# Performance work log

Hardware: AMD Instinct MI355X
Metric: run time of the kernel (lower is better)

The kernel has to match this reference:

```python
import jax, jax.numpy as jnp
import numpy as np

SPATIAL = ((100, 100), (50, 50), (25, 25), (13, 13))
STARTS = [0]
for _h, _w in SPATIAL[:-1]:
    STARTS.append(STARTS[-1] + _h * _w)
L_TOTAL = sum(h * w for h, w in SPATIAL)  # 13294
D, DFFN, NL, NH, NP = 256, 1024, 4, 8, 4
DH = D // NH
EPS = 1e-5


def _ln(x, g, b):
    mu = x.mean(-1, keepdims=True)
    var = ((x - mu) ** 2).mean(-1, keepdims=True)
    return (x - mu) * jax.lax.rsqrt(var + EPS) * g + b


def _bilinear(v_l, x, y, H, W):
    # v_l: [B,NH,H*W,DH]; x,y: [B,NH,Q*NP] pixel coords (grid_sample align_corners=False, zero padding)
    x0f = jnp.floor(x); y0f = jnp.floor(y)
    lx, ly = x - x0f, y - y0f
    x0 = x0f.astype(jnp.int32); y0 = y0f.astype(jnp.int32)
    acc = 0.0
    for dx, dy, w in ((0, 0, (1 - lx) * (1 - ly)), (1, 0, lx * (1 - ly)),
                      (0, 1, (1 - lx) * ly), (1, 1, lx * ly)):
        xi, yi = x0 + dx, y0 + dy
        valid = (xi >= 0) & (xi < W) & (yi >= 0) & (yi < H)
        idx = jnp.clip(yi, 0, H - 1) * W + jnp.clip(xi, 0, W - 1)
        g = jnp.take_along_axis(v_l, idx[..., None], axis=2)  # [B,NH,Q*NP,DH]
        acc = acc + g * (w * valid.astype(w.dtype))[..., None]
    return acc


def _msdeform(query, value_in, ref, norm_wh, Woff, boff, Wattn, battn, Wval, bval, Wout, bout):
    B, Q, _ = query.shape
    v = (value_in @ Wval + bval).reshape(B, L_TOTAL, NH, DH)
    off = (query @ Woff + boff).reshape(B, Q, NH, NL, NP, 2)
    aw = (query @ Wattn + battn).reshape(B, Q, NH, NL * NP)
    aw = jax.nn.softmax(aw, axis=-1).reshape(B, Q, NH, NL, NP)
    # normalized sampling locations in [0,1]: ref + offset / (W,H)
    loc = ref[:, :, None, :, None, :] + off / norm_wh[None, None, None, :, None, :]
    out = 0.0
    for l, (H, W) in enumerate(SPATIAL):
        s = STARTS[l]
        v_l = v[:, s:s + H * W].transpose(0, 2, 1, 3)          # [B,NH,HW,DH]
        loc_l = loc[:, :, :, l].transpose(0, 2, 1, 3, 4)       # [B,NH,Q,NP,2]
        x = (loc_l[..., 0] * W - 0.5).reshape(B, NH, Q * NP)
        y = (loc_l[..., 1] * H - 0.5).reshape(B, NH, Q * NP)
        samp = _bilinear(v_l, x, y, H, W).reshape(B, NH, Q, NP, DH)
        w_l = aw[:, :, :, l].transpose(0, 2, 1, 3)             # [B,NH,Q,NP]
        out = out + (samp * w_l[..., None]).sum(3)             # [B,NH,Q,DH]
    out = out.transpose(0, 2, 1, 3).reshape(B, Q, D)
    return out @ Wout + bout


def setup_inputs() -> dict:
    key = jax.random.key(0)
    ks = jax.random.split(key, 12)
    B = 4
    s = 0.02
    return {
        "src": jax.random.normal(ks[0], (B, L_TOTAL, D), jnp.float32),
        "pos": jax.random.normal(ks[1], (B, L_TOTAL, D), jnp.float32),
        "reference_points": jax.random.uniform(ks[2], (B, L_TOTAL, NL, 2), jnp.float32),
        "spatial_shapes": jnp.array(SPATIAL, jnp.int32),
        "level_start_index": jnp.array(STARTS, jnp.int32),
        "W_off": jax.random.normal(ks[3], (D, NH * NL * NP * 2), jnp.float32) * 0.01,
        "b_off": jax.random.normal(ks[4], (NH * NL * NP * 2,), jnp.float32) * 0.5,
        "W_attn": jax.random.normal(ks[5], (D, NH * NL * NP), jnp.float32) * s,
        "b_attn": jnp.zeros((NH * NL * NP,), jnp.float32),
        "W_val": jax.random.normal(ks[6], (D, D), jnp.float32) * s,
        "b_val": jnp.zeros((D,), jnp.float32),
        "W_out": jax.random.normal(ks[7], (D, D), jnp.float32) * s,
        "b_out": jnp.zeros((D,), jnp.float32),
        "ln_sa_g": jnp.ones((D,), jnp.float32),
        "ln_sa_b": jnp.zeros((D,), jnp.float32),
        "W1": jax.random.normal(ks[8], (D, DFFN), jnp.float32) * s,
        "b1": jnp.zeros((DFFN,), jnp.float32),
        "W2": jax.random.normal(ks[9], (DFFN, D), jnp.float32) * s,
        "b2": jnp.zeros((D,), jnp.float32),
        "ln_ff_g": jnp.ones((D,), jnp.float32),
        "ln_ff_b": jnp.zeros((D,), jnp.float32),
    }


def reference(src, pos, reference_points, spatial_shapes, level_start_index,
              W_off, b_off, W_attn, b_attn, W_val, b_val, W_out, b_out,
              ln_sa_g, ln_sa_b, W1, b1, W2, b2, ln_ff_g, ln_ff_b):
    # offset normalizer is (W, H) per level
    norm_wh = jnp.stack([spatial_shapes[:, 1], spatial_shapes[:, 0]], -1).astype(src.dtype)
    q = src + pos  # with_pos_embed
    sa = _msdeform(q, src, reference_points, norm_wh,
                   W_off, b_off, W_attn, b_attn, W_val, b_val, W_out, b_out)
    x = _ln(sa + src, ln_sa_g, ln_sa_b)          # dropout = identity (eval)
    y = jnp.maximum(x @ W1 + b1, 0.0) @ W2 + b2  # relu FFN
    return _ln(y + x, ln_ff_g, ln_ff_b)
```

## Files before the change

### kernel.cpp

```cpp
#include <hip/hip_runtime.h>
#include <hip/hip_bf16.h>

typedef __hip_bfloat16 bf16;
typedef short bf16x8 __attribute__((ext_vector_type(8)));
typedef float f32x4  __attribute__((ext_vector_type(4)));

#define ROWS 53176
#define LTOT 13294

__device__ __forceinline__ float b2f(bf16 v) { return __bfloat162float(v); }

__device__ __forceinline__ void gl2lds16(const void* g, void* l) {
    __builtin_amdgcn_global_load_lds(
        (const __attribute__((address_space(1))) unsigned*)g,
        (__attribute__((address_space(3))) unsigned*)l, 16, 0, 0);
}

template<bool RELU>
__global__ __launch_bounds__(256)
void mfma_gemm_n(const bf16* __restrict__ A, const bf16* __restrict__ Bt,
                 const float* __restrict__ bias, bf16* __restrict__ C,
                 int M, int N, int K)
{
    __shared__ __align__(16) short As[2][128 * 32];
    __shared__ __align__(16) short Bs[2][128 * 32];
    const int tid  = threadIdx.x;
    const int wave = tid >> 6, lane = tid & 63;

    const int nwg  = gridDim.x * gridDim.y;
    const int orig = blockIdx.y * gridDim.x + blockIdx.x;
    const int wgid = ((nwg & 7) == 0) ? ((orig & 7) * (nwg >> 3) + (orig >> 3)) : orig;
    const int bx = wgid % gridDim.x, by = wgid / gridDim.x;

    const int m0 = by * 128, n0 = bx * 128;
    const int lrow = lane >> 2, lcol = lane & 3;
    const int quad = lane >> 4, l15 = lane & 15;

    f32x4 acc[4][4];
#pragma unroll
    for (int i = 0; i < 4; ++i)
#pragma unroll
        for (int j = 0; j < 4; ++j) acc[i][j] = (f32x4){0.f, 0.f, 0.f, 0.f};

    const int wM = (wave >> 1) * 64, wN = (wave & 1) * 64;

    auto stage = [&](int p, int kk) {
#pragma unroll
        for (int q = 0; q < 2; ++q) {
            int rbase = wave * 32 + q * 16;
            int row = rbase + lrow;
            int sw = (lcol * 16) ^ ((row & 3) << 4);
            gl2lds16((const char*)(A  + (size_t)(m0 + row) * K + kk) + sw, &As[p][rbase * 32]);
            gl2lds16((const char*)(Bt + (size_t)(n0 + row) * K + kk) + sw, &Bs[p][rbase * 32]);
        }
    };

    auto compute = [&](int p) {
        bf16x8 af[4], bfr[4];
#pragma unroll
        for (int i = 0; i < 4; ++i) {
            int row = wM + i * 16 + l15;
            af[i] = *(const bf16x8*)((const char*)&As[p][row * 32]
                                     + ((quad * 16) ^ ((row & 3) << 4)));
        }
#pragma unroll
        for (int j = 0; j < 4; ++j) {
            int row = wN + j * 16 + l15;
            bfr[j] = *(const bf16x8*)((const char*)&Bs[p][row * 32]
                                      + ((quad * 16) ^ ((row & 3) << 4)));
        }
#pragma unroll
        for (int i = 0; i < 4; ++i)
#pragma unroll
            for (int j = 0; j < 4; ++j)
                acc[i][j] = __builtin_amdgcn_mfma_f32_16x16x32_bf16(bfr[j], af[i], acc[i][j], 0, 0, 0);
    };

    stage(0, 0);
    __syncthreads();
    int p = 0;
    for (int kk = 32; kk < K; kk += 32) {
        stage(p ^ 1, kk);
        compute(p);
        __syncthreads();
        p ^= 1;
    }
    compute(p);

    float4 b4[4];
#pragma unroll
    for (int j = 0; j < 4; ++j)
        b4[j] = *(const float4*)&bias[n0 + wN + j * 16 + quad * 4];

#pragma unroll
    for (int i = 0; i < 4; ++i) {
        int gm = m0 + wM + i * 16 + l15;
        if (gm >= M) continue;
#pragma unroll
        for (int j = 0; j < 4; ++j) {
            int gn = n0 + wN + j * 16 + quad * 4;
            union { bf16 h[4]; uint2 u2; } pk;
#pragma unroll
            for (int r = 0; r < 4; ++r) {
                float v = acc[i][j][r] + ((const float*)&b4[j])[r];
                if (RELU) v = fmaxf(v, 0.f);
                pk.h[r] = __float2bfloat16(v);
            }
            *(uint2*)&C[(size_t)gm * N + gn] = pk.u2;
        }
    }
}

template<typename OT>
__global__ __launch_bounds__(512)
void mfma_gemm_ln(const bf16* __restrict__ A, const bf16* __restrict__ Bt,
                  const float* __restrict__ bias, const bf16* __restrict__ res,
                  OT* __restrict__ C, const float* __restrict__ gam,
                  const float* __restrict__ bet, int M, int K)
{
    __shared__ __align__(16) short As[2][128 * 32];
    __shared__ __align__(16) short Bs[2][256 * 32];
    __shared__ float rsum[128], rsq[128];
    const int tid  = threadIdx.x;
    const int wave = tid >> 6, lane = tid & 63;
    const int m0 = blockIdx.x * 128;
    const int lrow = lane >> 2, lcol = lane & 3;
    const int quad = lane >> 4, l15 = lane & 15;
    if (tid < 128) { rsum[tid] = 0.f; rsq[tid] = 0.f; }

    f32x4 acc[4][4];
#pragma unroll
    for (int i = 0; i < 4; ++i)
#pragma unroll
        for (int j = 0; j < 4; ++j) acc[i][j] = (f32x4){0.f, 0.f, 0.f, 0.f};

    const int wM = (wave >> 2) * 64, wN = (wave & 3) * 64;

    auto stage = [&](int p, int kk) {
#pragma unroll
        for (int q = 0; q < 3; ++q) {
            int r = wave * 48 + q * 16;
            int sw;
            if (r < 128) {
                int row = r + lrow;
                sw = (lcol * 16) ^ ((row & 3) << 4);
                gl2lds16((const char*)(A + (size_t)(m0 + row) * K + kk) + sw, &As[p][r * 32]);
            } else {
                int rr = r - 128;
                int row = rr + lrow;
                sw = (lcol * 16) ^ ((row & 3) << 4);
                gl2lds16((const char*)(Bt + (size_t)(row) * K + kk) + sw, &Bs[p][rr * 32]);
            }
        }
    };

    auto compute = [&](int p) {
        bf16x8 af[4], bfr[4];
#pragma unroll
        for (int i = 0; i < 4; ++i) {
            int row = wM + i * 16 + l15;
            af[i] = *(const bf16x8*)((const char*)&As[p][row * 32]
                                     + ((quad * 16) ^ ((row & 3) << 4)));
        }
#pragma unroll
        for (int j = 0; j < 4; ++j) {
            int row = wN + j * 16 + l15;
            bfr[j] = *(const bf16x8*)((const char*)&Bs[p][row * 32]
                                      + ((quad * 16) ^ ((row & 3) << 4)));
        }
#pragma unroll
        for (int i = 0; i < 4; ++i)
#pragma unroll
            for (int j = 0; j < 4; ++j)
                acc[i][j] = __builtin_amdgcn_mfma_f32_16x16x32_bf16(bfr[j], af[i], acc[i][j], 0, 0, 0);
    };

    stage(0, 0);
    __syncthreads();
    int p = 0;
    for (int kk = 32; kk < K; kk += 32) {
        stage(p ^ 1, kk);
        compute(p);
        __syncthreads();
        p ^= 1;
    }
    compute(p);

    float4 b4[4], g4[4], be4[4];
#pragma unroll
    for (int j = 0; j < 4; ++j) {
        int gn = wN + j * 16 + quad * 4;
        b4[j]  = *(const float4*)&bias[gn];
        g4[j]  = *(const float4*)&gam[gn];
        be4[j] = *(const float4*)&bet[gn];
    }

    float lsum[4], lsq[4];
#pragma unroll
    for (int i = 0; i < 4; ++i) {
        int gm = m0 + wM + i * 16 + l15;
        lsum[i] = 0.f; lsq[i] = 0.f;
#pragma unroll
        for (int j = 0; j < 4; ++j) {
            int gn = wN + j * 16 + quad * 4;
            float r4[4] = {0.f, 0.f, 0.f, 0.f};
            if (gm < M) {
                uint2 ru = *(const uint2*)&res[(size_t)gm * 256 + gn];
                const bf16* rh = (const bf16*)&ru;
#pragma unroll
                for (int r = 0; r < 4; ++r) r4[r] = b2f(rh[r]);
            }
#pragma unroll
            for (int r = 0; r < 4; ++r) {
                float v = acc[i][j][r] + ((const float*)&b4[j])[r] + r4[r];
                acc[i][j][r] = v;
                lsum[i] += v;
                lsq[i]  += v * v;
            }
        }
#pragma unroll
        for (int mask = 16; mask <= 32; mask <<= 1) {
            lsum[i] += __shfl_xor(lsum[i], mask);
            lsq[i]  += __shfl_xor(lsq[i], mask);
        }
    }
    if (quad == 0) {
#pragma unroll
        for (int i = 0; i < 4; ++i) {
            atomicAdd(&rsum[wM + i * 16 + l15], lsum[i]);
            atomicAdd(&rsq [wM + i * 16 + l15], lsq[i]);
        }
    }
    __syncthreads();

#pragma unroll
    for (int i = 0; i < 4; ++i) {
        int lr = wM + i * 16 + l15;
        int gm = m0 + lr;
        if (gm >= M) continue;
        float mean = rsum[lr] * (1.f / 256.f);
        float var  = rsq[lr] * (1.f / 256.f) - mean * mean;
        float rstd = rsqrtf(fmaxf(var, 0.f) + 1e-5f);
#pragma unroll
        for (int j = 0; j < 4; ++j) {
            int gn = wN + j * 16 + quad * 4;
            if constexpr (sizeof(OT) == 2) {
                union { bf16 h[4]; uint2 u2; } pk;
#pragma unroll
                for (int r = 0; r < 4; ++r)
                    pk.h[r] = __float2bfloat16((acc[i][j][r] - mean) * rstd *
                              ((const float*)&g4[j])[r] + ((const float*)&be4[j])[r]);
                *(uint2*)&((bf16*)C)[(size_t)gm * 256 + gn] = pk.u2;
            } else {
                float4 o;
#pragma unroll
                for (int r = 0; r < 4; ++r)
                    ((float*)&o)[r] = (acc[i][j][r] - mean) * rstd *
                              ((const float*)&g4[j])[r] + ((const float*)&be4[j])[r];
                *(float4*)&((float*)C)[(size_t)gm * 256 + gn] = o;
            }
        }
    }
}

__global__ void cast_qs_kernel(const float* __restrict__ s, const float* __restrict__ p,
                               bf16* __restrict__ sb, bf16* __restrict__ qb, int n4)
{
    int i = blockIdx.x * 256 + threadIdx.x;
    if (i >= n4) return;
    float4 sv = ((const float4*)s)[i];
    float4 pv = ((const float4*)p)[i];
    union { bf16 h[4]; uint2 u; } a, b;
    a.h[0] = __float2bfloat16(sv.x); a.h[1] = __float2bfloat16(sv.y);
    a.h[2] = __float2bfloat16(sv.z); a.h[3] = __float2bfloat16(sv.w);
    b.h[0] = __float2bfloat16(sv.x + pv.x); b.h[1] = __float2bfloat16(sv.y + pv.y);
    b.h[2] = __float2bfloat16(sv.z + pv.z); b.h[3] = __float2bfloat16(sv.w + pv.w);
    ((uint2*)sb)[i] = a.u;
    ((uint2*)qb)[i] = b.u;
}

__global__ void wcast_all(const float* __restrict__ Wval, const float* __restrict__ Woff,
                          const float* __restrict__ Wattn, const float* __restrict__ Wout,
                          const float* __restrict__ W1, const float* __restrict__ W2,
                          const float* __restrict__ boff, const float* __restrict__ battn,
                          bf16* __restrict__ Wval_t, bf16* __restrict__ Wcat_t,
                          bf16* __restrict__ Wout_t, bf16* __restrict__ W1_t,
                          bf16* __restrict__ W2_t, float* __restrict__ bcat)
{
    int e = blockIdx.x * 256 + threadIdx.x;
    if (e < 384) bcat[e] = (e < 256) ? boff[e] : battn[e - 256];
    if (e < 65536) {
        int n = e >> 8, k = e & 255;
        Wval_t[e] = __float2bfloat16(Wval[k * 256 + n]);
    } else if (e < 163840) {
        int i = e - 65536; int n = i >> 8, k = i & 255;
        float w = (n < 256) ? Woff[k * 256 + n] : Wattn[k * 128 + (n - 256)];
        Wcat_t[i] = __float2bfloat16(w);
    } else if (e < 229376) {
        int i = e - 163840; int n = i >> 8, k = i & 255;
        Wout_t[i] = __float2bfloat16(Wout[k * 256 + n]);
    } else if (e < 491520) {
        int i = e - 229376; int n = i >> 8, k = i & 255;
        W1_t[i] = __float2bfloat16(W1[k * 1024 + n]);
    } else if (e < 753664) {
        int i = e - 491520; int n = i >> 10, k = i & 1023;
        W2_t[i] = __float2bfloat16(W2[k * 256 + n]);
    }
}

__global__ __launch_bounds__(256)
void sample_kernel(const bf16* __restrict__ v, const bf16* __restrict__ ocat,
                   const float* __restrict__ ref, bf16* __restrict__ samp)
{
    __shared__ int4 tab[64][33];
    const int tid = threadIdx.x;

    const int nwg = gridDim.x;
    const int orig = blockIdx.x;
    const int xcd = orig & 7, loc = orig >> 3;
    const int qn = nwg >> 3, rr = nwg & 7;
    const int bid = (xcd < rr ? xcd * (qn + 1) : rr * (qn + 1) + (xcd - rr) * qn) + loc;

    const int ps = tid >> 2;
    const int qt = tid & 3;
    const int gidx = bid * 64 + ps;
    const int h = gidx & 7, bq = gidx >> 3, b = bq / LTOT;

    {
        const int l = qt;
        const int W = (l == 0) ? 100 : (l == 1) ? 50 : (l == 2) ? 25 : 13;
        const int S = (l == 0) ? 0 : (l == 1) ? 10000 : (l == 2) ? 12500 : 13125;
        const float fW = (float)W;
        float rx = ref[(size_t)bq * 8 + l * 2 + 0];
        float ry = ref[(size_t)bq * 8 + l * 2 + 1];
        const bf16* ob = ocat + (size_t)bq * 384;
        float lg[4], ox[4], oy[4];
#pragma unroll
        for (int k = 0; k < 4; ++k) {
            ox[k] = b2f(ob[h * 32 + l * 8 + k * 2 + 0]);
            oy[k] = b2f(ob[h * 32 + l * 8 + k * 2 + 1]);
            lg[k] = b2f(ob[256 + h * 16 + l * 4 + k]);
        }
        float m = fmaxf(fmaxf(lg[0], lg[1]), fmaxf(lg[2], lg[3]));
        m = fmaxf(m, __shfl_xor(m, 1));
        m = fmaxf(m, __shfl_xor(m, 2));
        float ev[4]; float s = 0.f;
#pragma unroll
        for (int k = 0; k < 4; ++k) { ev[k] = __expf(lg[k] - m); s += ev[k]; }
        s += __shfl_xor(s, 1);
        s += __shfl_xor(s, 2);
        float inv = 1.f / s;
        const int base = (b * LTOT + S) * 512 + h * 64;
#pragma unroll
        for (int k = 0; k < 4; ++k) {
            float wgt = ev[k] * inv;
            float x = fmaf(rx, fW, ox[k] - 0.5f);
            float y = fmaf(ry, fW, oy[k] - 0.5f);
            float x0f = floorf(x), y0f = floorf(y);
            float lx = x - x0f, ly = y - y0f;
            int x0 = (int)x0f, y0 = (int)y0f;
            float tw[4] = {(1.f - lx) * (1.f - ly), lx * (1.f - ly),
                           (1.f - lx) * ly,         lx * ly};
            int o[4]; float w[4];
#pragma unroll
            for (int t = 0; t < 4; ++t) {
                int xi = x0 + (t & 1), yi = y0 + (t >> 1);
                bool ok = (xi >= 0) & (xi < W) & (yi >= 0) & (yi < W);
                o[t] = ok ? base + (yi * W + xi) * 512 : 0;
                w[t] = ok ? wgt * tw[t] : 0.f;
            }
            int e = (l * 4 + k) * 2;
            tab[ps][e + 0] = make_int4(o[0], __float_as_int(w[0]), o[1], __float_as_int(w[1]));
            tab[ps][e + 1] = make_int4(o[2], __float_as_int(w[2]), o[3], __float_as_int(w[3]));
        }
    }
    __syncthreads();

    const int lofs = qt * 16;
    const char* vc = (const char*)v;
    float al[4] = {0.f, 0.f, 0.f, 0.f}, ah[4] = {0.f, 0.f, 0.f, 0.f};
#pragma unroll 8
    for (int e2 = 0; e2 < 32; ++e2) {
        int4 q = tab[ps][e2];
        uint4 u0 = *(const uint4*)(vc + (size_t)(unsigned)(q.x + lofs));
        uint4 u1 = *(const uint4*)(vc + (size_t)(unsigned)(q.z + lofs));
        float w0 = __int_as_float(q.y), w1 = __int_as_float(q.w);
#pragma unroll
        for (int j = 0; j < 4; ++j) {
            unsigned e0 = ((const unsigned*)&u0)[j];
            unsigned e1 = ((const unsigned*)&u1)[j];
            al[j] += w0 * __uint_as_float(e0 << 16);
            ah[j] += w0 * __uint_as_float(e0);
            al[j] += w1 * __uint_as_float(e1 << 16);
            ah[j] += w1 * __uint_as_float(e1);
        }
    }
    union { unsigned u[4]; uint4 q; } r;
#pragma unroll
    for (int j = 0; j < 4; ++j) {
        union { struct { bf16 a, b; } h2; unsigned u; } t2;
        t2.h2.a = __float2bfloat16(al[j]);
        t2.h2.b = __float2bfloat16(ah[j]);
        r.u[j] = t2.u;
    }
    *(uint4*)((char*)samp + (size_t)gidx * 64 + lofs) = r.q;
}

extern "C" void kernel_launch(void* const* d_in, const int* in_sizes, int n_in,
                              void* d_out, int out_size, void* d_ws, size_t ws_size,
                              hipStream_t stream)
{
    const float* src     = (const float*)d_in[0];
    const float* pos     = (const float*)d_in[1];
    const float* ref     = (const float*)d_in[2];
    const float* W_off   = (const float*)d_in[5];
    const float* b_off   = (const float*)d_in[6];
    const float* W_attn  = (const float*)d_in[7];
    const float* b_attn  = (const float*)d_in[8];
    const float* W_val   = (const float*)d_in[9];
    const float* b_val   = (const float*)d_in[10];
    const float* W_out   = (const float*)d_in[11];
    const float* b_out   = (const float*)d_in[12];
    const float* ln_sa_g = (const float*)d_in[13];
    const float* ln_sa_b = (const float*)d_in[14];
    const float* W1      = (const float*)d_in[15];
    const float* b1      = (const float*)d_in[16];
    const float* W2      = (const float*)d_in[17];
    const float* b2      = (const float*)d_in[18];
    const float* ln_ff_g = (const float*)d_in[19];
    const float* ln_ff_b = (const float*)d_in[20];

    char* ws = (char*)d_ws;
    bf16* sb     = (bf16*)(ws);
    bf16* qb     = (bf16*)(ws + 27226112);
    bf16* samp   = (bf16*)(ws + 27226112);
    bf16* vbuf   = (bf16*)(ws + 54452224);
    bf16* ocat   = (bf16*)(ws + 81678336);
    bf16* xb16   = (bf16*)(ws + 122517504);
    bf16* hbuf   = (bf16*)(ws);
    bf16* Wval_t = (bf16*)(ws + 149743616);
    bf16* Wcat_t = (bf16*)(ws + 149874688);
    float* bcat  = (float*)(ws + 150071296);
    bf16* Wout_t = (bf16*)(ws + 150072832);
    bf16* W1_t   = (bf16*)(ws + 150203904);
    bf16* W2_t   = (bf16*)(ws + 150728192);
    float* outf  = (float*)d_out;

    dim3 blk(256);

    cast_qs_kernel<<<dim3((ROWS * 64 + 255) / 256), blk, 0, stream>>>(src, pos, sb, qb, ROWS * 64);
    wcast_all<<<dim3(2944), blk, 0, stream>>>(W_val, W_off, W_attn, W_out, W1, W2,
                                              b_off, b_attn,
                                              Wval_t, Wcat_t, Wout_t, W1_t, W2_t, bcat);

    mfma_gemm_n<false><<<dim3(2, 416), blk, 0, stream>>>(sb, Wval_t, b_val, vbuf, ROWS, 256, 256);
    mfma_gemm_n<false><<<dim3(3, 416), blk, 0, stream>>>(qb, Wcat_t, bcat, ocat, ROWS, 384, 256);
    sample_kernel<<<dim3(ROWS * 8 / 64), blk, 0, stream>>>(vbuf, ocat, ref, samp);
    mfma_gemm_ln<bf16><<<dim3(416), dim3(512), 0, stream>>>(
        samp, Wout_t, b_out, sb, xb16, ln_sa_g, ln_sa_b, ROWS, 256);
    mfma_gemm_n<true><<<dim3(8, 416), blk, 0, stream>>>(xb16, W1_t, b1, hbuf, ROWS, 1024, 256);
    mfma_gemm_ln<float><<<dim3(416), dim3(512), 0, stream>>>(
        hbuf, W2_t, b2, xb16, outf, ln_ff_g, ln_ff_b, ROWS, 1024);
}
```

Before: 468.8 us.

## Fuse value and offset GEMMs, store value head-major, merge cast kernels

Merges the value-projection and offset/attention GEMMs into one launch, with a workgroup-id swizzle that groups blocks sharing the same rows. The value output is written in a [B, head, pixel, 32] layout so each head's sampled pixels are contiguous, and the sampling table is reordered to iterate points before levels. It also fuses the activation cast and the weight cast/transpose into a single kernel. Together these cut launch count and are meant to improve gather locality in the sampler, at the cost of scattered 8-byte stores in the GEMM epilogue.

```diff
diff --git a/kernel.cpp b/kernel.cpp
--- a/kernel.cpp
+++ b/kernel.cpp
@@ -107,6 +107,113 @@
                 pk.h[r] = __float2bfloat16(v);
             }
             *(uint2*)&C[(size_t)gm * N + gn] = pk.u2;
+        }
+    }
+}
+
+__global__ __launch_bounds__(256)
+void mfma_gemm_vc(const bf16* __restrict__ Av, const bf16* __restrict__ Aq,
+                  const bf16* __restrict__ Bv, const bf16* __restrict__ Bc,
+                  const float* __restrict__ bv, const float* __restrict__ bc,
+                  bf16* __restrict__ Cv, bf16* __restrict__ Cc, int M)
+{
+    __shared__ __align__(16) short As[2][128 * 32];
+    __shared__ __align__(16) short Bs[2][128 * 32];
+    const int tid  = threadIdx.x;
+    const int wave = tid >> 6, lane = tid & 63;
+    const int K = 256;
+
+    const int nwg  = gridDim.x * gridDim.y;
+    const int orig = blockIdx.y * gridDim.x + blockIdx.x;
+    const int wgid = ((nwg & 7) == 0) ? ((orig & 7) * (nwg >> 3) + (orig >> 3)) : orig;
+    const int bx = wgid % gridDim.x, by = wgid / gridDim.x;
+
+    const bool isval = bx < 2;
+    const bf16* A    = isval ? Av : Aq;
+    const bf16* Bt   = isval ? Bv : Bc;
+    const float* bias = isval ? bv : bc;
+    const int n0 = isval ? bx * 128 : (bx - 2) * 128;
+
+    const int m0 = by * 128;
+    const int lrow = lane >> 2, lcol = lane & 3;
+    const int quad = lane >> 4, l15 = lane & 15;
+
+    f32x4 acc[4][4];
+#pragma unroll
+    for (int i = 0; i < 4; ++i)
+#pragma unroll
+        for (int j = 0; j < 4; ++j) acc[i][j] = (f32x4){0.f, 0.f, 0.f, 0.f};
+
+    const int wM = (wave >> 1) * 64, wN = (wave & 1) * 64;
+
+    auto stage = [&](int p, int kk) {
+#pragma unroll
+        for (int q = 0; q < 2; ++q) {
+            int rbase = wave * 32 + q * 16;
+            int row = rbase + lrow;
+            int sw = (lcol * 16) ^ ((row & 3) << 4);
+            gl2lds16((const char*)(A  + (size_t)(m0 + row) * K + kk) + sw, &As[p][rbase * 32]);
+            gl2lds16((const char*)(Bt + (size_t)(n0 + row) * K + kk) + sw, &Bs[p][rbase * 32]);
+        }
+    };
+
+    auto compute = [&](int p) {
+        bf16x8 af[4], bfr[4];
+#pragma unroll
+        for (int i = 0; i < 4; ++i) {
+            int row = wM + i * 16 + l15;
+            af[i] = *(const bf16x8*)((const char*)&As[p][row * 32]
+                                     + ((quad * 16) ^ ((row & 3) << 4)));
+        }
+#pragma unroll
+        for (int j = 0; j < 4; ++j) {
+            int row = wN + j * 16 + l15;
+            bfr[j] = *(const bf16x8*)((const char*)&Bs[p][row * 32]
+                                      + ((quad * 16) ^ ((row & 3) << 4)));
+        }
+#pragma unroll
+        for (int i = 0; i < 4; ++i)
+#pragma unroll
+            for (int j = 0; j < 4; ++j)
+                acc[i][j] = __builtin_amdgcn_mfma_f32_16x16x32_bf16(bfr[j], af[i], acc[i][j], 0, 0, 0);
+    };
+
+    stage(0, 0);
+    __syncthreads();
+    int p = 0;
+    for (int kk = 32; kk < K; kk += 32) {
+        stage(p ^ 1, kk);
+        compute(p);
+        __syncthreads();
+        p ^= 1;
+    }
+    compute(p);
+
+    float4 b4[4];
+#pragma unroll
+    for (int j = 0; j < 4; ++j)
+        b4[j] = *(const float4*)&bias[n0 + wN + j * 16 + quad * 4];
+
+#pragma unroll
+    for (int i = 0; i < 4; ++i) {
+        int gm = m0 + wM + i * 16 + l15;
+        if (gm >= M) continue;
+        int b   = gm / LTOT;
+        int pix = gm - b * LTOT;
+#pragma unroll
+        for (int j = 0; j < 4; ++j) {
+            int gn = n0 + wN + j * 16 + quad * 4;
+            union { bf16 h[4]; uint2 u2; } pk;
+#pragma unroll
+            for (int r = 0; r < 4; ++r)
+                pk.h[r] = __float2bfloat16(acc[i][j][r] + ((const float*)&b4[j])[r]);
+            if (isval) {
+                int head = gn >> 5, ch = gn & 31;
+                size_t idx = ((size_t)(b * 8 + head) * LTOT + pix) * 32 + ch;
+                *(uint2*)&Cv[idx] = pk.u2;
+            } else {
+                *(uint2*)&Cc[(size_t)gm * 384 + gn] = pk.u2;
+            }
         }
     }
 }
@@ -263,31 +370,32 @@
     }
 }
 
-__global__ void cast_qs_kernel(const float* __restrict__ s, const float* __restrict__ p,
-                               bf16* __restrict__ sb, bf16* __restrict__ qb, int n4)
+__global__ __launch_bounds__(256)
+void cast_all(const float* __restrict__ s, const float* __restrict__ p,
+              bf16* __restrict__ sb, bf16* __restrict__ qb,
+              const float* __restrict__ Wval, const float* __restrict__ Woff,
+              const float* __restrict__ Wattn, const float* __restrict__ Wout,
+              const float* __restrict__ W1, const float* __restrict__ W2,
+              const float* __restrict__ boff, const float* __restrict__ battn,
+              bf16* __restrict__ Wval_t, bf16* __restrict__ Wcat_t,
+              bf16* __restrict__ Wout_t, bf16* __restrict__ W1_t,
+              bf16* __restrict__ W2_t, float* __restrict__ bcat)
 {
-    int i = blockIdx.x * 256 + threadIdx.x;
-    if (i >= n4) return;
-    float4 sv = ((const float4*)s)[i];
-    float4 pv = ((const float4*)p)[i];
-    union { bf16 h[4]; uint2 u; } a, b;
-    a.h[0] = __float2bfloat16(sv.x); a.h[1] = __float2bfloat16(sv.y);
-    a.h[2] = __float2bfloat16(sv.z); a.h[3] = __float2bfloat16(sv.w);
-    b.h[0] = __float2bfloat16(sv.x + pv.x); b.h[1] = __float2bfloat16(sv.y + pv.y);
-    b.h[2] = __float2bfloat16(sv.z + pv.z); b.h[3] = __float2bfloat16(sv.w + pv.w);
-    ((uint2*)sb)[i] = a.u;
-    ((uint2*)qb)[i] = b.u;
-}
-
-__global__ void wcast_all(const float* __restrict__ Wval, const float* __restrict__ Woff,
-                          const float* __restrict__ Wattn, const float* __restrict__ Wout,
-                          const float* __restrict__ W1, const float* __restrict__ W2,
-                          const float* __restrict__ boff, const float* __restrict__ battn,
-                          bf16* __restrict__ Wval_t, bf16* __restrict__ Wcat_t,
-                          bf16* __restrict__ Wout_t, bf16* __restrict__ W1_t,
-                          bf16* __restrict__ W2_t, float* __restrict__ bcat)
-{
-    int e = blockIdx.x * 256 + threadIdx.x;
+    const int blk = blockIdx.x;
+    if (blk < 13294) {
+        int i = blk * 256 + threadIdx.x;
+        float4 sv = ((const float4*)s)[i];
+        float4 pv = ((const float4*)p)[i];
+        union { bf16 h[4]; uint2 u; } a, b;
+        a.h[0] = __float2bfloat16(sv.x); a.h[1] = __float2bfloat16(sv.y);
+        a.h[2] = __float2bfloat16(sv.z); a.h[3] = __float2bfloat16(sv.w);
+        b.h[0] = __float2bfloat16(sv.x + pv.x); b.h[1] = __float2bfloat16(sv.y + pv.y);
+        b.h[2] = __float2bfloat16(sv.z + pv.z); b.h[3] = __float2bfloat16(sv.w + pv.w);
+        ((uint2*)sb)[i] = a.u;
+        ((uint2*)qb)[i] = b.u;
+        return;
+    }
+    int e = (blk - 13294) * 256 + threadIdx.x;
     if (e < 384) bcat[e] = (e < 256) ? boff[e] : battn[e - 256];
     if (e < 65536) {
         int n = e >> 8, k = e & 255;
@@ -350,7 +458,7 @@
         s += __shfl_xor(s, 1);
         s += __shfl_xor(s, 2);
         float inv = 1.f / s;
-        const int base = (b * LTOT + S) * 512 + h * 64;
+        const int base = ((b * 8 + h) * LTOT + S) * 64;
 #pragma unroll
         for (int k = 0; k < 4; ++k) {
             float wgt = ev[k] * inv;
@@ -366,10 +474,10 @@
             for (int t = 0; t < 4; ++t) {
                 int xi = x0 + (t & 1), yi = y0 + (t >> 1);
                 bool ok = (xi >= 0) & (xi < W) & (yi >= 0) & (yi < W);
-                o[t] = ok ? base + (yi * W + xi) * 512 : 0;
+                o[t] = ok ? base + (yi * W + xi) * 64 : 0;
                 w[t] = ok ? wgt * tw[t] : 0.f;
             }
-            int e = (l * 4 + k) * 2;
+            int e = k * 8 + l * 2;
             tab[ps][e + 0] = make_int4(o[0], __float_as_int(w[0]), o[1], __float_as_int(w[1]));
             tab[ps][e + 1] = make_int4(o[2], __float_as_int(w[2]), o[3], __float_as_int(w[3]));
         }
@@ -448,13 +556,13 @@
 
     dim3 blk(256);
 
-    cast_qs_kernel<<<dim3((ROWS * 64 + 255) / 256), blk, 0, stream>>>(src, pos, sb, qb, ROWS * 64);
-    wcast_all<<<dim3(2944), blk, 0, stream>>>(W_val, W_off, W_attn, W_out, W1, W2,
+    cast_all<<<dim3(16238), blk, 0, stream>>>(src, pos, sb, qb,
+                                              W_val, W_off, W_attn, W_out, W1, W2,
                                               b_off, b_attn,
                                               Wval_t, Wcat_t, Wout_t, W1_t, W2_t, bcat);
 
-    mfma_gemm_n<false><<<dim3(2, 416), blk, 0, stream>>>(sb, Wval_t, b_val, vbuf, ROWS, 256, 256);
-    mfma_gemm_n<false><<<dim3(3, 416), blk, 0, stream>>>(qb, Wcat_t, bcat, ocat, ROWS, 384, 256);
+    mfma_gemm_vc<<<dim3(5, 416), blk, 0, stream>>>(sb, qb, Wval_t, Wcat_t,
+                                                   b_val, bcat, vbuf, ocat, ROWS);
     sample_kernel<<<dim3(ROWS * 8 / 64), blk, 0, stream>>>(vbuf, ocat, ref, samp);
     mfma_gemm_ln<bf16><<<dim3(416), dim3(512), 0, stream>>>(
         samp, Wout_t, b_out, sb, xb16, ln_sa_g, ln_sa_b, ROWS, 256);
```

After: 518.8 us. 1.11x slower.
